# Performance work log

Hardware: AMD Instinct MI355X
Metric: run time of the kernel (lower is better)

## Reference

```python
import jax, jax.numpy as jnp
import numpy as np

N_NODES = 50000
N_EDGES = 1600000
IN_DIM = 128
OUT_DIM = 16
N_HEADS = 8


def setup_inputs() -> dict:
    key = jax.random.key(0)
    ks = jax.random.split(key, 9)
    s = 1.0 / np.sqrt(IN_DIM)
    return {
        "h": jax.random.normal(ks[0], (N_NODES, IN_DIM), jnp.float32),
        "Wq": jax.random.normal(ks[1], (IN_DIM, OUT_DIM * N_HEADS), jnp.float32) * s,
        "bq": jax.random.normal(ks[2], (OUT_DIM * N_HEADS,), jnp.float32) * 0.01,
        "Wk": jax.random.normal(ks[3], (IN_DIM, OUT_DIM * N_HEADS), jnp.float32) * s,
        "bk": jax.random.normal(ks[4], (OUT_DIM * N_HEADS,), jnp.float32) * 0.01,
        "Wv": jax.random.normal(ks[5], (IN_DIM, OUT_DIM * N_HEADS), jnp.float32) * s,
        "bv": jax.random.normal(ks[6], (OUT_DIM * N_HEADS,), jnp.float32) * 0.01,
        "src": jax.random.randint(ks[7], (N_EDGES,), 0, N_NODES, jnp.int32),
        "dst": jax.random.randint(ks[8], (N_EDGES,), 0, N_NODES, jnp.int32),
    }


def reference(h, Wq, bq, Wk, bk, Wv, bv, src, dst):
    n_nodes = h.shape[0]
    # node-wise Q/K/V projections -> [N, H, D]
    Q = (h @ Wq + bq).reshape(n_nodes, N_HEADS, OUT_DIM)
    K = (h @ Wk + bk).reshape(n_nodes, N_HEADS, OUT_DIM)
    V = (h @ Wv + bv).reshape(n_nodes, N_HEADS, OUT_DIM)
    # edge-wise score: (K[src] * Q[dst]).sum(-1), scaled-exp with clamp
    score = jnp.sum(K[src] * Q[dst], axis=-1)  # [E, H]
    score = jnp.exp(jnp.clip(score / np.sqrt(OUT_DIM), -5.0, 5.0))
    # scatter-sum weighted values and normalizers to dst nodes
    msg = V[src] * score[:, :, None]  # [E, H, D]
    wV = jax.ops.segment_sum(msg, dst, num_segments=n_nodes)  # [N, H, D]
    z = jax.ops.segment_sum(score, dst, num_segments=n_nodes)  # [N, H]
    return wV / (z[:, :, None] + 1e-6)
```

## Files before the change

### kernel.cpp

```cpp
#include <hip/hip_runtime.h>
#include <hip/hip_bf16.h>
#include <cstddef>

#define N_NODES 50000
#define N_EDGES 1600000
#define IN_DIM 128
#define OUT_DIM 16
#define N_HEADS 8
#define QKV_DIM 128
#define HS_STRIDE 136
#define OS_STRIDE 392

#define SUBB 3125
#define BCAP 1024
#define BH_CHUNK 8192
#define BH_BLOCKS 196
#define GEMM_BLOCKS 782
#define FUSED_BLOCKS (BH_BLOCKS + GEMM_BLOCKS)

typedef __hip_bfloat16 bf16;
typedef short bf16x8 __attribute__((ext_vector_type(8)));
typedef float f32x4  __attribute__((ext_vector_type(4)));

__device__ __forceinline__ float b2f(bf16 x) { return __bfloat162float(x); }

__device__ __forceinline__ float u16tof(unsigned int u) {
    unsigned int x = u << 16;
    float f;
    __builtin_memcpy(&f, &x, 4);
    return f;
}

__device__ __forceinline__ unsigned short f2bf(float v) {
    bf16 b = __float2bfloat16(v);
    unsigned short u;
    __builtin_memcpy(&u, &b, 2);
    return u;
}

__global__ __launch_bounds__(256) void sentinel_kernel(unsigned short* __restrict__ out, int n) {
    int i = blockIdx.x * 256 + threadIdx.x;
    if (i < n) out[i] = 0x42C8;
}

__global__ __launch_bounds__(256) void prep_kernel(
    const unsigned short* __restrict__ hraw,
    const void* __restrict__ Wqr, const void* __restrict__ bqr,
    const void* __restrict__ Wkr, const void* __restrict__ bkr,
    const void* __restrict__ Wvr, const void* __restrict__ bvr,
    int* __restrict__ flag,
    unsigned short* __restrict__ Wfrag, float* __restrict__ bias_f)
{
    __shared__ int red[256];
    const int t   = threadIdx.x;
    const int tid = blockIdx.x * 256 + t;

    int cnt = 0;
    for (int i = t; i < 8192; i += 256) {
        unsigned short u = hraw[i];
        int e = (u >> 7) & 0xFF;
        if (e == 0xFF || e > 0x85 || (e == 0 && (u & 0x7F) != 0)) cnt++;
    }
    red[t] = cnt;
    __syncthreads();
    for (int s = 128; s > 0; s >>= 1) {
        if (t < s) red[t] += red[t + s];
        __syncthreads();
    }
    const bool f32 = (red[0] > 100);
    if (blockIdx.x == 0 && t == 0) *flag = red[0];

    if (tid < 384) {
        int mat = tid >> 7, c = tid & 127;
        const void* bp = (mat == 0) ? bqr : (mat == 1) ? bkr : bvr;
        bias_f[tid] = f32 ? ((const float*)bp)[c] : b2f(((const bf16*)bp)[c]);
    }

    int l  = tid & 63;
    int s  = (tid >> 6) & 3;
    int nt = tid >> 8;
    int n  = nt * 16 + (l & 15);
    int k0 = s * 32 + (l >> 4) * 8;
    int mat = n >> 7, c = n & 127;
    const void* Wp = (mat == 0) ? Wqr : (mat == 1) ? Wkr : Wvr;

    unsigned short v[8];
#pragma unroll
    for (int j = 0; j < 8; ++j) {
        int k = k0 + j;
        float w = f32 ? ((const float*)Wp)[k * QKV_DIM + c]
                      : b2f(((const bf16*)Wp)[k * QKV_DIM + c]);
        v[j] = f2bf(w);
    }
    ushort4* o = (ushort4*)(Wfrag + (size_t)tid * 8);
    o[0] = make_ushort4(v[0], v[1], v[2], v[3]);
    o[1] = make_ushort4(v[4], v[5], v[6], v[7]);
}

__global__ __launch_bounds__(256) void fused_gs_kernel(
    const void* __restrict__ hraw,
    const unsigned short* __restrict__ Wfrag, const float* __restrict__ bias_f,
    const int* __restrict__ flag,
    unsigned short* __restrict__ Qt, unsigned short* __restrict__ KVt,
    const int* __restrict__ src, const int* __restrict__ dst,
    unsigned int* __restrict__ packed, unsigned int* __restrict__ offcnt)
{
    __shared__ __align__(16) unsigned char arena[64 * OS_STRIDE * 2];
    const int t = threadIdx.x;

    if (blockIdx.x < BH_BLOCKS) {
        int* lcnt           = (int*)arena;
        unsigned int* stage = (unsigned int*)(arena + 12544);
        int* sm             = (int*)(arena + 45312);
        int* carryp         = (int*)(arena + 46336);

        const int b    = blockIdx.x;
        const int base = b * BH_CHUNK;
        const int nb   = min(N_EDGES - base, BH_CHUNK);

        for (int i = t; i < SUBB; i += 256) lcnt[i] = 0;
        if (t == 0) *carryp = 0;
        __syncthreads();

        for (int i = t; i < nb; i += 256)
            atomicAdd(&lcnt[dst[base + i] >> 4], 1);
        __syncthreads();

        for (int c = 0; c < 13; ++c) {
            int i = c * 256 + t;
            int x = (i < SUBB) ? lcnt[i] : 0;
            int v = x;
            sm[t] = v;
            __syncthreads();
            for (int s = 1; s < 256; s <<= 1) {
                int a = (t >= s) ? sm[t - s] : 0;
                __syncthreads();
                v += a;
                sm[t] = v;
                __syncthreads();
            }
            int off = *carryp + v - x;
            if (i < SUBB) {
                offcnt[(size_t)b * SUBB + i] =
                    ((unsigned int)off << 16) | (unsigned int)x;
                lcnt[i] = off;
            }
            __syncthreads();
            if (t == 255) *carryp += v;
            __syncthreads();
        }

        for (int i = t; i < nb; i += 256) {
            int d = dst[base + i];
            int bk = d >> 4;
            int pos = atomicAdd(&lcnt[bk], 1);
            stage[pos] = (unsigned int)src[base + i] | ((unsigned int)(d & 15) << 16);
        }
        __syncthreads();

        for (int i = t; i < nb; i += 256)
            packed[base + i] = stage[i];

    } else {
        unsigned short* smem = (unsigned short*)arena;

        const bool f32 = (*flag > 100);
        const int m0 = (blockIdx.x - BH_BLOCKS) * 64;

#pragma unroll
        for (int it = 0; it < 8; ++it) {
            int idx = it * 1024 + t * 4;
            int r = idx >> 7, k = idx & 127;
            int row = m0 + r;
            ushort4 w4 = make_ushort4(0, 0, 0, 0);
            if (row < N_NODES) {
                if (f32) {
                    float4 v4 = ((const float4*)hraw)[(size_t)row * 32 + (k >> 2)];
                    w4 = make_ushort4(f2bf(v4.x), f2bf(v4.y), f2bf(v4.z), f2bf(v4.w));
                } else {
                    uint2 u = ((const uint2*)hraw)[(size_t)row * 32 + (k >> 2)];
                    w4 = make_ushort4((unsigned short)(u.x & 0xffffu), (unsigned short)(u.x >> 16),
                                      (unsigned short)(u.y & 0xffffu), (unsigned short)(u.y >> 16));
                }
            }
            *(ushort4*)&smem[r * HS_STRIDE + k] = w4;
        }
        __syncthreads();

        const int lane = t & 63;
        const int wave = t >> 6;
        const int qd   = lane >> 4;
        const int ln15 = lane & 15;

        bf16x8 afr[4][4];
#pragma unroll
        for (int ms = 0; ms < 4; ++ms)
#pragma unroll
            for (int s = 0; s < 4; ++s)
                afr[ms][s] = *(const bf16x8*)&smem[(ms * 16 + ln15) * HS_STRIDE + s * 32 + qd * 8];

        __syncthreads();

#pragma unroll
        for (int i = 0; i < 6; ++i) {
            const int nt  = wave + i * 4;
            const int col = nt * 16 + ln15;
            const float bs = bias_f[col];
            const int mat = col >> 7, c127 = col & 127;
            const int ocol = (mat == 0) ? c127
                           : 128 + 8 * (c127 >> 2) + (c127 & 3) + ((mat == 2) ? 4 : 0);

            bf16x8 bfr[4];
#pragma unroll
            for (int s = 0; s < 4; ++s)
                bfr[s] = *(const bf16x8*)(Wfrag + ((size_t)(nt * 4 + s) * 64 + lane) * 8);

#pragma unroll
            for (int ms = 0; ms < 4; ++ms) {
                f32x4 acc = {0.f, 0.f, 0.f, 0.f};
#pragma unroll
                for (int s = 0; s < 4; ++s)
                    acc = __builtin_amdgcn_mfma_f32_16x16x32_bf16(afr[ms][s], bfr[s], acc, 0, 0, 0);
#pragma unroll
                for (int r = 0; r < 4; ++r) {
                    int rl = ms * 16 + qd * 4 + r;
                    smem[rl * OS_STRIDE + ocol] = f2bf(acc[r] + bs);
                }
            }
        }
        __syncthreads();

        for (int q = t; q < 1024; q += 256) {
            int row = q >> 4, c = q & 15;
            int grow = m0 + row;
            if (grow < N_NODES)
                ((uint4*)Qt)[grow * 16 + c] = *(const uint4*)&smem[row * OS_STRIDE + c * 8];
        }
        for (int q = t; q < 2048; q += 256) {
            int row = q >> 5, g = q & 31;
            int grow = m0 + row;
            if (grow < N_NODES)
                ((uint4*)KVt)[grow * 32 + g] = *(const uint4*)&smem[row * OS_STRIDE + 128 + g * 8];
        }
    }
}

__global__ __launch_bounds__(256) void bucket_agg_kernel(
    const unsigned short* __restrict__ Qt, const unsigned short* __restrict__ KVt,
    const unsigned int* __restrict__ packed, const unsigned int* __restrict__ offcnt,
    const int* __restrict__ flag, void* __restrict__ out)
{
    __shared__ unsigned int   lds_pk[BCAP];
    __shared__ unsigned short lds_src[BCAP];
    __shared__ int runoff[BH_BLOCKS], runcnt[BH_BLOCKS], runpfx[BH_BLOCKS];
    __shared__ int cnt16[16], base16[16], cur16[16];
    __shared__ int nb_s;

    const int sb = blockIdx.x;
    const int t  = threadIdx.x;

    if (t < 16) { cnt16[t] = 0; cur16[t] = 0; }
    if (t < BH_BLOCKS) {
        unsigned int oc = offcnt[(size_t)t * SUBB + sb];
        runoff[t] = t * BH_CHUNK + (int)(oc >> 16);
        runcnt[t] = (int)(oc & 0xffffu);
    }
    __syncthreads();

    {
        int* sm = (int*)lds_pk;
        int x = (t < BH_BLOCKS) ? runcnt[t] : 0;
        int v = x;
        sm[t] = v;
        __syncthreads();
        for (int s = 1; s < 256; s <<= 1) {
            int a = (t >= s) ? sm[t - s] : 0;
            __syncthreads();
            v += a;
            sm[t] = v;
            __syncthreads();
        }
        if (t < BH_BLOCKS) runpfx[t] = v - x;
        if (t == 255) nb_s = v;
        __syncthreads();
    }
    const int nb = min(nb_s, BCAP);

    for (int r = t; r < BH_BLOCKS; r += 256) {
        int ro = runoff[r], rc = runcnt[r], rp = runpfx[r];
        for (int j = 0; j < rc; ++j) {
            int dpos = rp + j;
            if (dpos < BCAP) {
                unsigned int pk = packed[ro + j];
                lds_pk[dpos] = pk;
                atomicAdd(&cnt16[(pk >> 16) & 15], 1);
            }
        }
    }
    __syncthreads();
    if (t == 0) {
        int acc = 0;
#pragma unroll
        for (int i = 0; i < 16; ++i) { base16[i] = acc; acc += cnt16[i]; }
    }
    __syncthreads();
    for (int j = t; j < nb; j += 256) {
        unsigned int pk = lds_pk[j];
        int dl = (pk >> 16) & 15;
        int pos = base16[dl] + atomicAdd(&cur16[dl], 1);
        lds_src[pos] = (unsigned short)(pk & 0xffffu);
    }
    __syncthreads();

    const int wave = t >> 6;
    const int lane = t & 63;
    const int half = lane >> 5;
    const int hl   = lane & 31;
    const uint4* KV4 = (const uint4*)KVt;
    const bool of32 = (*flag > 100);

    for (int dl = wave; dl < 16; dl += 4) {
        const int d = sb * 16 + dl;
        uint2 qw = ((const uint2*)Qt)[d * 32 + hl];
        const float q0 = u16tof(qw.x & 0xffffu), q1 = u16tof(qw.x >> 16);
        const float q2 = u16tof(qw.y & 0xffffu), q3 = u16tof(qw.y >> 16);
        const int off = base16[dl];
        const int n   = cnt16[dl];

        float a0 = 0.f, a1 = 0.f, a2 = 0.f, a3 = 0.f, zz = 0.f;

#define CONSUME(KV, SCMASK)                                                     \
        {                                                                       \
            float p = fmaf(u16tof((KV).x & 0xffffu), q0,                        \
                      fmaf(u16tof((KV).x >> 16), q1,                            \
                      fmaf(u16tof((KV).y & 0xffffu), q2,                        \
                           u16tof((KV).y >> 16) * q3)));                        \
            p += __shfl_xor(p, 1);                                              \
            p += __shfl_xor(p, 2);                                              \
            float sc = __expf(__builtin_amdgcn_fmed3f(p * 0.25f, -5.f, 5.f));   \
            sc *= (SCMASK);                                                     \
            a0 = fmaf(u16tof((KV).z & 0xffffu), sc, a0);                        \
            a1 = fmaf(u16tof((KV).z >> 16),     sc, a1);                        \
            a2 = fmaf(u16tof((KV).w & 0xffffu), sc, a2);                        \
            a3 = fmaf(u16tof((KV).w >> 16),     sc, a3);                        \
            zz += sc;                                                           \
        }

        int j = 0;
        for (; j + 8 <= n; j += 8) {
            int e[4];
#pragma unroll
            for (int u = 0; u < 4; ++u) e[u] = lds_src[off + j + 2 * u + half];
            uint4 kv[4];
#pragma unroll
            for (int u = 0; u < 4; ++u) kv[u] = KV4[e[u] * 32 + hl];
#pragma unroll
            for (int u = 0; u < 4; ++u) CONSUME(kv[u], 1.f)
        }
        for (; j + 2 <= n; j += 2) {
            int e = lds_src[off + j + half];
            uint4 kv = KV4[e * 32 + hl];
            CONSUME(kv, 1.f)
        }
        if (j < n) {
            int e = lds_src[off + j];
            uint4 kv = KV4[e * 32 + hl];
            CONSUME(kv, (half == 0) ? 1.f : 0.f)
        }
#undef CONSUME

        a0 += __shfl_xor(a0, 32);
        a1 += __shfl_xor(a1, 32);
        a2 += __shfl_xor(a2, 32);
        a3 += __shfl_xor(a3, 32);
        zz += __shfl_xor(zz, 32);

        const float inv = 1.f / (zz + 1e-6f);
        const float r0 = a0 * inv, r1 = a1 * inv, r2 = a2 * inv, r3 = a3 * inv;

        if (half == 0) {
            if (of32) {
                ((float4*)out)[d * 32 + hl] = make_float4(r0, r1, r2, r3);
            } else {
                unsigned int w0 = ((unsigned int)f2bf(r1) << 16) | f2bf(r0);
                unsigned int w1 = ((unsigned int)f2bf(r3) << 16) | f2bf(r2);
                ((uint2*)out)[d * 32 + hl] = make_uint2(w0, w1);
            }
        }
    }
}

extern "C" void kernel_launch(void* const* d_in, const int* in_sizes, int n_in,
                              void* d_out, int out_size, void* d_ws, size_t ws_size,
                              hipStream_t stream)
{
    const void* h  = d_in[0];
    const void* Wq = d_in[1];
    const void* bq = d_in[2];
    const void* Wk = d_in[3];
    const void* bk = d_in[4];
    const void* Wv = d_in[5];
    const void* bv = d_in[6];
    const int*  src = (const int*)d_in[7];
    const int*  dst = (const int*)d_in[8];

    const size_t NQ = (size_t)N_NODES * QKV_DIM;
    const size_t WFRAG_N = 24 * 4 * 64 * 8;
    const size_t PACKED_N = (size_t)BH_BLOCKS * BH_CHUNK;
    const size_t OFFCNT_N = (size_t)BH_BLOCKS * SUBB;

    const size_t need = 3 * NQ * 2 + WFRAG_N * 2 + 384 * 4 + 64
                      + PACKED_N * 4 + OFFCNT_N * 4;

    if (ws_size < need) {
        sentinel_kernel<<<(out_size + 255) / 256, 256, 0, stream>>>((unsigned short*)d_out, out_size);
        return;
    }

    unsigned short* Qt  = (unsigned short*)d_ws;
    unsigned short* KVt = Qt + NQ;
    unsigned short* Wfrag = KVt + 2 * NQ;
    float* bias_f = (float*)(Wfrag + WFRAG_N);
    int* flag     = (int*)(bias_f + 384);
    unsigned int* packed = (unsigned int*)(flag + 16);
    unsigned int* offcnt = packed + PACKED_N;

    prep_kernel<<<24, 256, 0, stream>>>((const unsigned short*)h,
        Wq, bq, Wk, bk, Wv, bv, flag, Wfrag, bias_f);

    fused_gs_kernel<<<FUSED_BLOCKS, 256, 0, stream>>>(h, Wfrag, bias_f, flag,
        Qt, KVt, src, dst, packed, offcnt);

    bucket_agg_kernel<<<SUBB, 256, 0, stream>>>(Qt, KVt, packed, offcnt, flag, d_out);
}
```

Before: 265.4 us.

## Use wave-shuffle scan, larger bucket chunks, and direct scatter in bucketing

The block-level Hillis-Steele scan over the bucket counts, which needed many __syncthreads per 256-wide chunk, is replaced by a per-wave shuffle scan plus a small second-level scan of the chunk totals. Each bucketing block now handles twice as many edges, so there are half as many blocks and half as many per-block offset tables. The LDS staging buffer is dropped and edges are scattered straight to global memory. This trades coalesced global writes for scattered ones and gives each block more serial work while the GEMM blocks run alongside it. Downstream code that reads offcnt must also handle the new chunk size and the larger offsets, which the hidden code may or may not do.

```diff
diff --git a/kernel.cpp b/kernel.cpp
--- a/kernel.cpp
+++ b/kernel.cpp
@@ -12,9 +12,11 @@
 #define OS_STRIDE 392
 
 #define SUBB 3125
+#define SUBB_PAD 3136
+#define NCHUNK 49
 #define BCAP 1024
-#define BH_CHUNK 8192
-#define BH_BLOCKS 196
+#define BH_CHUNK 16384
+#define BH_BLOCKS 98
 #define GEMM_BLOCKS 782
 #define FUSED_BLOCKS (BH_BLOCKS + GEMM_BLOCKS)
 
@@ -109,57 +111,66 @@
     const int t = threadIdx.x;
 
     if (blockIdx.x < BH_BLOCKS) {
-        int* lcnt           = (int*)arena;
-        unsigned int* stage = (unsigned int*)(arena + 12544);
-        int* sm             = (int*)(arena + 45312);
-        int* carryp         = (int*)(arena + 46336);
+        int* lcnt = (int*)arena;
+        int* sc   = (int*)(arena + 12544);
+        int* ctot = (int*)(arena + 25088);
+        int* cpfx = (int*)(arena + 25344);
 
         const int b    = blockIdx.x;
         const int base = b * BH_CHUNK;
         const int nb   = min(N_EDGES - base, BH_CHUNK);
-
-        for (int i = t; i < SUBB; i += 256) lcnt[i] = 0;
-        if (t == 0) *carryp = 0;
+        const int wave = t >> 6;
+        const int lane = t & 63;
+
+        for (int i = t; i < SUBB_PAD; i += 256) lcnt[i] = 0;
         __syncthreads();
 
         for (int i = t; i < nb; i += 256)
             atomicAdd(&lcnt[dst[base + i] >> 4], 1);
         __syncthreads();
 
-        for (int c = 0; c < 13; ++c) {
-            int i = c * 256 + t;
+        for (int c = wave; c < NCHUNK; c += 4) {
+            int i = c * 64 + lane;
             int x = (i < SUBB) ? lcnt[i] : 0;
             int v = x;
-            sm[t] = v;
-            __syncthreads();
-            for (int s = 1; s < 256; s <<= 1) {
-                int a = (t >= s) ? sm[t - s] : 0;
-                __syncthreads();
-                v += a;
-                sm[t] = v;
-                __syncthreads();
-            }
-            int off = *carryp + v - x;
-            if (i < SUBB) {
+#pragma unroll
+            for (int s = 1; s < 64; s <<= 1) {
+                int a = __shfl_up(v, s);
+                if (lane >= s) v += a;
+            }
+            sc[i] = v;
+            if (lane == 63) ctot[c] = v;
+        }
+        __syncthreads();
+
+        if (wave == 0) {
+            int x = (lane < NCHUNK) ? ctot[lane] : 0;
+            int v = x;
+#pragma unroll
+            for (int s = 1; s < 64; s <<= 1) {
+                int a = __shfl_up(v, s);
+                if (lane >= s) v += a;
+            }
+            if (lane < NCHUNK) cpfx[lane] = v - x;
+        }
+        __syncthreads();
+
+        for (int i = t; i < SUBB_PAD; i += 256) {
+            int x    = lcnt[i];
+            int excl = cpfx[i >> 6] + sc[i] - x;
+            if (i < SUBB)
                 offcnt[(size_t)b * SUBB + i] =
-                    ((unsigned int)off << 16) | (unsigned int)x;
-                lcnt[i] = off;
-            }
-            __syncthreads();
-            if (t == 255) *carryp += v;
-            __syncthreads();
-        }
+                    ((unsigned int)excl << 16) | (unsigned int)x;
+            lcnt[i] = excl;
+        }
+        __syncthreads();
 
         for (int i = t; i < nb; i += 256) {
-            int d = dst[base + i];
+            int d  = dst[base + i];
             int bk = d >> 4;
             int pos = atomicAdd(&lcnt[bk], 1);
-            stage[pos] = (unsigned int)src[base + i] | ((unsigned int)(d & 15) << 16);
-        }
-        __syncthreads();
-
-        for (int i = t; i < nb; i += 256)
-            packed[base + i] = stage[i];
+            packed[base + pos] = (unsigned int)src[base + i] | ((unsigned int)(d & 15) << 16);
+        }
 
     } else {
         unsigned short* smem = (unsigned short*)arena;
```

Measured after the change: 294.5 us. 11.0% more time.
